# Performance work log

Hardware: AMD Instinct MI355X
Metric: run time of the kernel (lower is better)

## Reference

```python
import jax, jax.numpy as jnp
import numpy as np
import math

SIG = 0.3989422804014327  # 1/sqrt(2*pi): makes sqrt_pi == 1, matching init_kwargs
N = 4000002


def _toeplitz_like_t(c):
    # Faithful result of toeplitz_like(x,5).t() for x=[1,N]:
    # full Toeplitz T[i,j]=c[|i-j|], narrow(1,0,2).narrow(0,1,N-2).t()
    # => rows are shifted windows c[1:N-1] and c[0:N-2], shape [2, N-2].
    n = c.shape[0]
    return jnp.stack([c[1:n - 1], c[0:n - 2]], axis=0)


def _component(A, B, log_sqrt_pi):
    # A, B: [M, D].  sum_{i,j,k} exp(-0.5*(A[i,k]-B[j,k])^2/sig^2)/sqrt_pi / (M*M)
    M = A.shape[0]
    diff = A[:, None, :] - B[None, :, :]          # [M, M, D]
    g = jnp.exp(-0.5 * (diff * diff) / (SIG * SIG) - log_sqrt_pi)
    return jnp.sum(g) / (M * M)


def setup_inputs() -> dict:
    key = jax.random.key(0)
    k1, k2 = jax.random.split(key)
    d = jax.random.normal(k1, (N,), dtype=jnp.float32)
    y = jax.random.normal(k2, (N,), dtype=jnp.float32)
    return {"d": d, "y": y}


def reference(d, y):
    Dm = _toeplitz_like_t(d)                      # [2, N-2]
    Ym = _toeplitz_like_t(y)                      # [2, N-2]
    Ddim = Ym.shape[1]
    # sqrt_pi = sqrt((2*pi)^D * sig^(2D)); computed stably in log space
    log_sqrt_pi = 0.5 * Ddim * (math.log(2.0 * math.pi) + 2.0 * math.log(SIG))
    log_sqrt_pi = jnp.float32(log_sqrt_pi)
    same_y = _component(Ym, Ym, log_sqrt_pi)
    same_d = _component(Dm, Dm, log_sqrt_pi)
    combined = -2.0 * _component(Dm, Ym, log_sqrt_pi)
    return same_y + same_d + combined
```

## Files before the change

### kernel.cpp

```cpp
#include <hip/hip_runtime.h>


#define PI_F 3.14159265358979323846f

__global__ __launch_bounds__(256) void casamento_kernel(
    const float* __restrict__ d, const float* __restrict__ y,
    float* __restrict__ out, int D)
{
    int tid = blockIdx.x * blockDim.x + threadIdx.x;
    int stride = gridDim.x * blockDim.x;

    float acc = 0.0f;
    for (int k = tid; k < D; k += stride) {
        float d0 = d[k], d1 = d[k + 1];
        float y0 = y[k], y1 = y[k + 1];

        float dy = y1 - y0;
        float dd = d1 - d0;
        float c00 = d1 - y1;
        float c01 = d1 - y0;
        float c10 = d0 - y1;
        float c11 = d0 - y0;

        float t = __expf(-PI_F * dy * dy) + __expf(-PI_F * dd * dd)
                - __expf(-PI_F * c00 * c00) - __expf(-PI_F * c01 * c01)
                - __expf(-PI_F * c10 * c10) - __expf(-PI_F * c11 * c11);
        acc += 0.5f * t;
    }

    for (int off = 32; off > 0; off >>= 1)
        acc += __shfl_down(acc, off, 64);

    __shared__ float warp_sums[4];
    int lane = threadIdx.x & 63;
    int wid  = threadIdx.x >> 6;
    if (lane == 0) warp_sums[wid] = acc;
    __syncthreads();

    if (threadIdx.x == 0) {
        float s = warp_sums[0] + warp_sums[1] + warp_sums[2] + warp_sums[3];
        if (blockIdx.x == 0) s += (float)D;
        atomicAdd(out, s);
    }
}

extern "C" void kernel_launch(void* const* d_in, const int* in_sizes, int n_in,
                              void* d_out, int out_size, void* d_ws, size_t ws_size,
                              hipStream_t stream) {
    const float* d = (const float*)d_in[0];
    const float* y = (const float*)d_in[1];
    float* out = (float*)d_out;

    int N = in_sizes[0];
    int D = N - 2;

    hipMemsetAsync(out, 0, sizeof(float), stream);

    const int block = 256;
    const int grid = 1024;
    casamento_kernel<<<grid, block, 0, stream>>>(d, y, out, D);
}
```

Baseline: 89.84 us.

## Vectorize loads with float4 and launch one thread per four elements

Each thread now loads float4 chunks of d and y plus one halo element and evaluates four consecutive window terms. The grid-stride loop over 1024 blocks is replaced by a grid sized to cover all elements once, with a scalar tail handled by thread 0. This cuts load instruction count and loop overhead. In exchange it launches about 3900 blocks, each issuing an atomicAdd, which adds atomic contention on the single output.

```diff
diff --git a/kernel.cpp b/kernel.cpp
--- a/kernel.cpp
+++ b/kernel.cpp
@@ -3,30 +3,45 @@
 
 #define PI_F 3.14159265358979323846f
 
+__device__ __forceinline__ float six_terms(float d0, float d1, float y0, float y1) {
+    float dy = y1 - y0;
+    float dd = d1 - d0;
+    float c00 = d1 - y1;
+    float c01 = d1 - y0;
+    float c10 = d0 - y1;
+    float c11 = d0 - y0;
+    return __expf(-PI_F * dy * dy) + __expf(-PI_F * dd * dd)
+         - __expf(-PI_F * c00 * c00) - __expf(-PI_F * c01 * c01)
+         - __expf(-PI_F * c10 * c10) - __expf(-PI_F * c11 * c11);
+}
+
 __global__ __launch_bounds__(256) void casamento_kernel(
     const float* __restrict__ d, const float* __restrict__ y,
     float* __restrict__ out, int D)
 {
-    int tid = blockIdx.x * blockDim.x + threadIdx.x;
-    int stride = gridDim.x * blockDim.x;
+    int gid = blockIdx.x * blockDim.x + threadIdx.x;
+    int D4 = D >> 2;
+    float acc = 0.0f;
 
-    float acc = 0.0f;
-    for (int k = tid; k < D; k += stride) {
-        float d0 = d[k], d1 = d[k + 1];
-        float y0 = y[k], y1 = y[k + 1];
+    if (gid < D4) {
+        int base = gid << 2;
+        float4 dv = *(const float4*)(d + base);
+        float4 yv = *(const float4*)(y + base);
+        float d4 = d[base + 4];
+        float y4 = y[base + 4];
 
-        float dy = y1 - y0;
-        float dd = d1 - d0;
-        float c00 = d1 - y1;
-        float c01 = d1 - y0;
-        float c10 = d0 - y1;
-        float c11 = d0 - y0;
+        acc += six_terms(dv.x, dv.y, yv.x, yv.y);
+        acc += six_terms(dv.y, dv.z, yv.y, yv.z);
+        acc += six_terms(dv.z, dv.w, yv.z, yv.w);
+        acc += six_terms(dv.w, d4,   yv.w, y4);
+    }
 
-        float t = __expf(-PI_F * dy * dy) + __expf(-PI_F * dd * dd)
-                - __expf(-PI_F * c00 * c00) - __expf(-PI_F * c01 * c01)
-                - __expf(-PI_F * c10 * c10) - __expf(-PI_F * c11 * c11);
-        acc += 0.5f * t;
+    if (gid == 0) {
+        for (int k = (D4 << 2); k < D; ++k)
+            acc += six_terms(d[k], d[k + 1], y[k], y[k + 1]);
     }
+
+    acc *= 0.5f;
 
     for (int off = 32; off > 0; off >>= 1)
         acc += __shfl_down(acc, off, 64);
@@ -53,10 +68,12 @@
 
     int N = in_sizes[0];
     int D = N - 2;
+    int D4 = D >> 2;
 
     hipMemsetAsync(out, 0, sizeof(float), stream);
 
     const int block = 256;
-    const int grid = 1024;
+    int grid = (D4 + block - 1) / block;
+    if (grid < 1) grid = 1;
     casamento_kernel<<<grid, block, 0, stream>>>(d, y, out, D);
 }
```

Result: slower. 121.1 us (+34.8%).
